# Kernel tuning notes

Hardware: AMD Instinct MI355X
Metric: run time of the kernel (lower is better)

## Reference

```python
import jax, jax.numpy as jnp
import numpy as np

DIM = 768
HID = 3072  # 4 * DIM
EPS = 1e-5


def layer_norm(x, w, b):
    mu = jnp.mean(x, axis=-1, keepdims=True)
    var = jnp.var(x, axis=-1, keepdims=True)
    return (x - mu) * jax.lax.rsqrt(var + EPS) * w + b


def setup_inputs() -> dict:
    key = jax.random.key(0)
    ks = jax.random.split(key, 8)
    C, H = DIM, HID
    s = lambda fan_in: 1.0 / np.sqrt(fan_in)
    return {
        "x": jax.random.normal(ks[0], (32, 577, C), dtype=jnp.float32),
        "norm1_w": jnp.ones((C,), jnp.float32),
        "norm1_b": jnp.zeros((C,), jnp.float32),
        "qkv_w": jax.random.uniform(ks[1], (3 * C, C), jnp.float32, -s(C), s(C)),
        "proj_w": jax.random.uniform(ks[2], (C, C), jnp.float32, -s(C), s(C)),
        "proj_b": jax.random.uniform(ks[3], (C,), jnp.float32, -s(C), s(C)),
        "norm2_w": jnp.ones((C,), jnp.float32),
        "norm2_b": jnp.zeros((C,), jnp.float32),
        "fc1_w": jax.random.uniform(ks[4], (H, C), jnp.float32, -s(C), s(C)),
        "fc1_b": jax.random.uniform(ks[5], (H,), jnp.float32, -s(C), s(C)),
        "fc2_w": jax.random.uniform(ks[6], (C, H), jnp.float32, -s(H), s(H)),
        "fc2_b": jax.random.uniform(ks[7], (C,), jnp.float32, -s(H), s(H)),
    }


def reference(x, norm1_w, norm1_b, qkv_w, proj_w, proj_b,
              norm2_w, norm2_b, fc1_w, fc1_b, fc2_w, fc2_b):
    B, N, C = x.shape
    attn_size = int((N - 1) ** 0.5)
    scale = C ** -0.5

    # --- Attention on norm1(x) (single head) ---
    h = layer_norm(x, norm1_w, norm1_b)
    qkv = (h @ qkv_w.T).reshape(B, N, 3, C)           # [B,N,3,C]
    q, k, v = qkv[:, :, 0], qkv[:, :, 1], qkv[:, :, 2]
    attn = jax.nn.softmax(jnp.einsum('bnc,bmc->bnm', q, k) * scale, axis=-1)
    y = jnp.einsum('bnm,bmc->bnc', attn, v)           # [B,N,C]
    # Faithful to torch: .transpose(1,2).reshape(B,N,C) scrambles layout
    y = jnp.transpose(y, (0, 2, 1)).reshape(B, N, C)
    a = y @ proj_w.T + proj_b
    token_attn = attn[:, 0, 1:].reshape(B, 1, attn_size, attn_size)

    # Faithful to torch Block: input residual is discarded, attention out doubled
    x = a + a

    # --- MLP (exact GELU, as nn.GELU default) ---
    m = layer_norm(x, norm2_w, norm2_b)
    m = jax.nn.gelu(m @ fc1_w.T + fc1_b, approximate=False)
    m = m @ fc2_w.T + fc2_b
    x = x + m
    return (x, token_attn)
```

## Files before the change

### kernel.cpp

```cpp
#include <hip/hip_runtime.h>
#include <hip/hip_bf16.h>

#define Bz   32
#define Nn_  577
#define Np   640
#define Cc   768
#define Hh   3072
#define Mrows (Bz * Nn_)
#define OUT_X (Mrows * Cc)
#define SCALE 0.03608439182435161f

typedef unsigned short ushort_t;
typedef short short8 __attribute__((ext_vector_type(8)));
typedef float f32x4 __attribute__((ext_vector_type(4)));

__device__ __forceinline__ ushort_t f2b(float f) {
    __hip_bfloat16 h = __float2bfloat16(f);
    return *reinterpret_cast<ushort_t*>(&h);
}

__device__ __forceinline__ void gl16(const ushort_t* g, ushort_t* l) {
    __builtin_amdgcn_global_load_lds(
        (const __attribute__((address_space(1))) void*)g,
        (__attribute__((address_space(3))) void*)l, 16, 0, 0);
}

__device__ __forceinline__ float bsum(float v, float* sm) {
    #pragma unroll
    for (int o = 32; o > 0; o >>= 1) v += __shfl_down(v, o, 64);
    int lane = threadIdx.x & 63, wid = threadIdx.x >> 6;
    if (lane == 0) sm[wid] = v;
    __syncthreads();
    float r = sm[0] + sm[1] + sm[2] + sm[3];
    __syncthreads();
    return r;
}
__device__ __forceinline__ float bmax(float v, float* sm) {
    #pragma unroll
    for (int o = 32; o > 0; o >>= 1) v = fmaxf(v, __shfl_down(v, o, 64));
    int lane = threadIdx.x & 63, wid = threadIdx.x >> 6;
    if (lane == 0) sm[wid] = v;
    __syncthreads();
    float r = fmaxf(fmaxf(sm[0], sm[1]), fmaxf(sm[2], sm[3]));
    __syncthreads();
    return r;
}

__global__ void cvt_kernel(const float* __restrict__ in, ushort_t* __restrict__ out, int n) {
    int i = blockIdx.x * 256 + threadIdx.x;
    if (i < n) out[i] = f2b(in[i]);
}

__global__ void ln_bf16(const float* __restrict__ x, const float* __restrict__ w,
                        const float* __restrict__ b, ushort_t* __restrict__ out) {
    __shared__ float sm[8];
    long long row = blockIdx.x;
    const float* xr = x + row * Cc;
    float v[3]; float s = 0.f;
    #pragma unroll
    for (int i = 0; i < 3; ++i) { v[i] = xr[threadIdx.x + i * 256]; s += v[i]; }
    float mu = bsum(s, sm) * (1.f / (float)Cc);
    float sq = 0.f;
    #pragma unroll
    for (int i = 0; i < 3; ++i) { float d = v[i] - mu; sq += d * d; }
    float var = bsum(sq, sm + 4) * (1.f / (float)Cc);
    float inv = rsqrtf(var + 1e-5f);
    ushort_t* orow = out + row * Cc;
    #pragma unroll
    for (int i = 0; i < 3; ++i) {
        int c = threadIdx.x + i * 256;
        orow[c] = f2b((v[i] - mu) * inv * w[c] + b[c]);
    }
}

__global__ void softmax_bf16(const float* __restrict__ Sf, ushort_t* __restrict__ Sb,
                             float* __restrict__ tok) {
    __shared__ float sm[8];
    long long row = blockIdx.x;
    int b_l = (int)(row / Nn_), r = (int)(row - (long long)b_l * Nn_);
    const float* src = Sf + row * Np;
    ushort_t* dst = Sb + row * Np;
    float v[3]; float mx = -1e30f;
    #pragma unroll
    for (int i = 0; i < 3; ++i) {
        int c = threadIdx.x + i * 256;
        v[i] = (c < Nn_) ? src[c] : -1e30f;
        mx = fmaxf(mx, v[i]);
    }
    mx = bmax(mx, sm);
    float s = 0.f;
    #pragma unroll
    for (int i = 0; i < 3; ++i) {
        int c = threadIdx.x + i * 256;
        v[i] = (c < Nn_) ? expf(v[i] - mx) : 0.f;
        s += v[i];
    }
    s = bsum(s, sm + 4);
    float inv = 1.f / s;
    #pragma unroll
    for (int i = 0; i < 3; ++i) {
        int c = threadIdx.x + i * 256;
        float p = v[i] * inv;
        if (c < Np) dst[c] = (c < Nn_) ? f2b(p) : (ushort_t)0;
        if (r == 0 && c >= 1 && c < Nn_) tok[(long long)b_l * 576 + (c - 1)] = p;
    }
}

#define EPS_STORE  0
#define EPS_X2     1
#define EPS_GELU   2
#define EPS_ADD    3
#define EPS_QKV    4

#define MM_STAGE(AS, BS, k0) do {            \
    gl16(Ag0 + (k0), &AS[e0]);               \
    gl16(Ag1 + (k0), &AS[e1]);               \
    gl16(Bg0 + (k0), &BS[e0]);               \
    gl16(Bg1 + (k0), &BS[e1]);               \
} while (0)

#define MM_COMPUTE(AS, BS) do {                                             \
    short8 af[4], bfr[4];                                                   \
    _Pragma("unroll")                                                       \
    for (int i = 0; i < 4; ++i) {                                           \
        int r = wr + i * 16 + fr;                                           \
        af[i] = *(const short8*)&AS[r * 32 + ((kq ^ (r & 3)) << 3)];        \
    }                                                                       \
    _Pragma("unroll")                                                       \
    for (int j = 0; j < 4; ++j) {                                           \
        int r = wc + j * 16 + fr;                                           \
        bfr[j] = *(const short8*)&BS[r * 32 + ((kq ^ (r & 3)) << 3)];       \
    }                                                                       \
    _Pragma("unroll")                                                       \
    for (int i = 0; i < 4; ++i)                                             \
        _Pragma("unroll")                                                   \
        for (int j = 0; j < 4; ++j)                                         \
            acc[i][j] = __builtin_amdgcn_mfma_f32_16x16x32_bf16(            \
                af[i], bfr[j], acc[i][j], 0, 0, 0);                         \
} while (0)

template<int EPI, typename OutT>
__global__ __launch_bounds__(256)
void mm_bf16(const ushort_t* __restrict__ A, long long sAb, int lda, int M,
             const ushort_t* __restrict__ B, long long sBb, int ldb, int Nv,
             const float* __restrict__ bias,
             OutT* __restrict__ O, long long sOb, int ldo,
             int K, float alpha,
             ushort_t* __restrict__ qQ, ushort_t* __restrict__ qK, ushort_t* __restrict__ qV)
{
    __shared__ __align__(16) ushort_t As0[128 * 32];
    __shared__ __align__(16) ushort_t As1[128 * 32];
    __shared__ __align__(16) ushort_t Bs0[128 * 32];
    __shared__ __align__(16) ushort_t Bs1[128 * 32];
    const int z = blockIdx.z;
    A += (long long)z * sAb; B += (long long)z * sBb;
    if (O) O += (long long)z * sOb;
    const int n0 = blockIdx.x * 128;
    const int m0 = blockIdx.y * 128;
    const int tid = threadIdx.x;
    const int lane = tid & 63;
    const int wv = tid >> 6;
    const int wr = (wv >> 1) << 6;
    const int wc = (wv & 1) << 6;
    const int fr = lane & 15;
    const int kq = lane >> 4;

    const int e0 = tid * 8, e1 = 2048 + tid * 8;
    const int ra0 = e0 >> 5, qa0 = (((e0 & 31) >> 3) ^ (ra0 & 3)) << 3;
    const int ra1 = e1 >> 5, qa1 = (((e1 & 31) >> 3) ^ (ra1 & 3)) << 3;
    const ushort_t* Ag0 = A + (long long)min(m0 + ra0, M - 1) * lda + qa0;
    const ushort_t* Ag1 = A + (long long)min(m0 + ra1, M - 1) * lda + qa1;
    const ushort_t* Bg0 = B + (long long)min(n0 + ra0, Nv - 1) * ldb + qa0;
    const ushort_t* Bg1 = B + (long long)min(n0 + ra1, Nv - 1) * ldb + qa1;

    f32x4 acc[4][4] = {};

    const int nt = K >> 5;

    MM_STAGE(As0, Bs0, 0);
    __syncthreads();

    for (int t = 0; t < nt; t += 2) {
        MM_STAGE(As1, Bs1, (t + 1) << 5);
        MM_COMPUTE(As0, Bs0);
        __syncthreads();
        if (t + 2 < nt) MM_STAGE(As0, Bs0, (t + 2) << 5);
        MM_COMPUTE(As1, Bs1);
        __syncthreads();
    }

    #pragma unroll
    for (int i = 0; i < 4; ++i) {
        int mb = m0 + wr + i * 16 + (lane >> 4) * 4;
        #pragma unroll
        for (int j = 0; j < 4; ++j) {
            int n = n0 + wc + j * 16 + fr;
            if (n >= Nv) continue;
            f32x4 v4 = acc[i][j];
            #pragma unroll
            for (int r = 0; r < 4; ++r) {
                int m = mb + r;
                if (m >= M) continue;
                float v = v4[r] * alpha;
                if constexpr (EPI == EPS_QKV) {
                    int b_l = m / Nn_, rr = m - b_l * Nn_;
                    if (n < Cc)            qQ[(long long)m * Cc + n] = f2b(v);
                    else if (n < 2 * Cc)   qK[(long long)m * Cc + (n - Cc)] = f2b(v);
                    else                   qV[((long long)b_l * Cc + (n - 2 * Cc)) * Np + rr] = f2b(v);
                } else if constexpr (EPI == EPS_ADD) {
                    if (bias) v += bias[n];
                    long long oi = (long long)m * ldo + n;
                    O[oi] += v;
                } else {
                    if (bias) v += bias[n];
                    if constexpr (EPI == EPS_X2) v *= 2.f;
                    if constexpr (EPI == EPS_GELU) v = 0.5f * v * (1.f + erff(v * 0.70710678118654752f));
                    long long oi = (long long)m * ldo + n;
                    if constexpr (sizeof(OutT) == 2) O[oi] = (OutT)f2b(v);
                    else                             O[oi] = (OutT)v;
                }
            }
        }
    }
}

extern "C" void kernel_launch(void* const* d_in, const int* in_sizes, int n_in,
                              void* d_out, int out_size, void* d_ws, size_t ws_size,
                              hipStream_t stream) {
    const float* x      = (const float*)d_in[0];
    const float* n1w    = (const float*)d_in[1];
    const float* n1b    = (const float*)d_in[2];
    const float* qkv_w  = (const float*)d_in[3];
    const float* proj_w = (const float*)d_in[4];
    const float* proj_b = (const float*)d_in[5];
    const float* n2w    = (const float*)d_in[6];
    const float* n2b    = (const float*)d_in[7];
    const float* fc1w   = (const float*)d_in[8];
    const float* fc1b   = (const float*)d_in[9];
    const float* fc2w   = (const float*)d_in[10];
    const float* fc2b   = (const float*)d_in[11];
    float* out = (float*)d_out;
    float* x2  = out;
    float* tok = out + OUT_X;

    char* ws = (char*)d_ws;
    const long long nWq = (long long)3 * Cc * Cc;
    const long long nWp = (long long)Cc * Cc;
    const long long nW1 = (long long)Hh * Cc;
    const long long nW2 = (long long)Cc * Hh;
    ushort_t* wq = (ushort_t*)ws;
    ushort_t* wp = wq + nWq;
    ushort_t* w1 = wp + nWp;
    ushort_t* w2 = w1 + nW1;
    const long long WBYTES = 2 * (nWq + nWp + nW1 + nW2);
    char* dyn = ws + WBYTES;
    long long avail = (long long)ws_size - WBYTES;

    const long long perG = 3LL * Nn_ * Cc * 2 + (long long)Cc * Np * 2
                         + (long long)Nn_ * Np * 4 + (long long)Nn_ * Np * 2;
    int G = 1;
    { const int o[6] = {32, 16, 8, 4, 2, 1};
      for (int i = 0; i < 6; ++i) if ((long long)o[i] * perG <= avail) { G = o[i]; break; } }
    int CH = Nn_;
    { const int o[6] = {32, 16, 8, 4, 2, 1};
      for (int i = 0; i < 6; ++i) if ((long long)o[i] * Nn_ * (Cc + Hh) * 2 <= avail) { CH = o[i] * Nn_; break; } }

    ushort_t* hbf = (ushort_t*)dyn;
    ushort_t* Q   = hbf + (long long)G * Nn_ * Cc;
    ushort_t* Kb  = Q   + (long long)G * Nn_ * Cc;
    ushort_t* Vt  = Kb  + (long long)G * Nn_ * Cc;
    float*    Sf  = (float*)(Vt + (long long)G * Cc * Np);
    ushort_t* Sb  = (ushort_t*)(Sf + (long long)G * Nn_ * Np);
    ushort_t* Yt  = hbf;
    ushort_t* g = (ushort_t*)dyn;
    ushort_t* t = g + (long long)CH * Cc;

    cvt_kernel<<<(int)((nWq + 255) / 256), 256, 0, stream>>>(qkv_w, wq, (int)nWq);
    cvt_kernel<<<(int)((nWp + 255) / 256), 256, 0, stream>>>(proj_w, wp, (int)nWp);
    cvt_kernel<<<(int)((nW1 + 255) / 256), 256, 0, stream>>>(fc1w, w1, (int)nW1);
    cvt_kernel<<<(int)((nW2 + 255) / 256), 256, 0, stream>>>(fc2w, w2, (int)nW2);

    for (int b0 = 0; b0 < Bz; b0 += G) {
        const int MR = G * Nn_;
        const int myM = (MR + 127) / 128;

        ln_bf16<<<MR, 256, 0, stream>>>(x + (long long)b0 * Nn_ * Cc, n1w, n1b, hbf);

        mm_bf16<EPS_QKV, float><<<dim3(18, myM, 1), 256, 0, stream>>>(
            hbf, 0, Cc, MR, wq, 0, Cc, 3 * Cc, nullptr,
            (float*)nullptr, 0, 0, Cc, 1.f, Q, Kb, Vt);

        mm_bf16<EPS_STORE, float><<<dim3(5, 5, G), 256, 0, stream>>>(
            Q, (long long)Nn_ * Cc, Cc, Nn_, Kb, (long long)Nn_ * Cc, Cc, Nn_, nullptr,
            Sf, (long long)Nn_ * Np, Np, Cc, SCALE, nullptr, nullptr, nullptr);

        softmax_bf16<<<MR, 256, 0, stream>>>(Sf, Sb, tok + (long long)b0 * 576);

        mm_bf16<EPS_STORE, ushort_t><<<dim3(5, 6, G), 256, 0, stream>>>(
            Vt, (long long)Cc * Np, Np, Cc, Sb, (long long)Nn_ * Np, Np, Nn_, nullptr,
            Yt, (long long)Cc * Nn_, Nn_, Np, 1.f, nullptr, nullptr, nullptr);

        mm_bf16<EPS_X2, float><<<dim3(6, myM, 1), 256, 0, stream>>>(
            Yt, 0, Cc, MR, wp, 0, Cc, Cc, proj_b,
            x2 + (long long)b0 * Nn_ * Cc, 0, Cc, Cc, 1.f, nullptr, nullptr, nullptr);
    }

    for (int c0 = 0; c0 < Mrows; c0 += CH) {
        const int cn = (Mrows - c0 < CH) ? (Mrows - c0) : CH;
        const int myC = (cn + 127) / 128;

        ln_bf16<<<cn, 256, 0, stream>>>(x2 + (long long)c0 * Cc, n2w, n2b, g);

        mm_bf16<EPS_GELU, ushort_t><<<dim3(24, myC, 1), 256, 0, stream>>>(
            g, 0, Cc, cn, w1, 0, Cc, Hh, fc1b,
            t, 0, Hh, Cc, 1.f, nullptr, nullptr, nullptr);

        mm_bf16<EPS_ADD, float><<<dim3(6, myC, 1), 256, 0, stream>>>(
            t, 0, Hh, cn, w2, 0, Hh, Cc, fc2b,
            x2 + (long long)c0 * Cc, 0, Cc, Hh, 1.f, nullptr, nullptr, nullptr);
    }
}
```

Baseline: 890.0 us.

## Add 256x256 double-buffered MFMA GEMM kernel for dense projections

Introduces mm256, a 512-thread GEMM with 256x256 output tiles and two LDS buffers. Global-to-LDS loads for the next K tile are issued before computing the current one, with a swizzled LDS layout, s_setprio around the MFMA bursts and an XCD-aware workgroup remap. It replaces the 128-tile mm_bf16 for the QKV, proj, fc1 and fc2 GEMMs to raise data reuse per tile and overlap loads with compute. In exchange it uses 128KB of LDS per block, limiting occupancy to one block per CU, and launches far fewer workgroups, which can leave CUs underused on the smaller GEMMs.

Result: faster. 872.1 us (-2.0%).

```diff
diff --git a/kernel.cpp b/kernel.cpp
--- a/kernel.cpp
+++ b/kernel.cpp
@@ -224,6 +224,144 @@
     }
 }
 
+#define STAGE256(LA, LB, kt) do {                                   \
+    _Pragma("unroll")                                               \
+    for (int j = 0; j < 4; ++j) gl16(Ag[j] + (kt) * 64, &LA[j * 4096 + sdst]); \
+    _Pragma("unroll")                                               \
+    for (int j = 0; j < 4; ++j) gl16(Bg[j] + (kt) * 64, &LB[j * 4096 + sdst]); \
+} while (0)
+
+#define COMPUTE256(LA, LB) do {                                                   \
+    short8 bfv[4][2];                                                             \
+    _Pragma("unroll")                                                             \
+    for (int nf = 0; nf < 4; ++nf) {                                              \
+        int rb = (wn64 + nf * 16 + fr) * 64;                                      \
+        bfv[nf][0] = *(const short8*)&LB[rb + ck0];                               \
+        bfv[nf][1] = *(const short8*)&LB[rb + ck1];                               \
+    }                                                                             \
+    _Pragma("unroll")                                                             \
+    for (int mh = 0; mh < 4; ++mh) {                                              \
+        int ra0 = (wm128 + mh * 32 + fr) * 64;                                    \
+        int ra1 = (wm128 + mh * 32 + 16 + fr) * 64;                               \
+        short8 a00 = *(const short8*)&LA[ra0 + ck0];                              \
+        short8 a01 = *(const short8*)&LA[ra0 + ck1];                              \
+        short8 a10 = *(const short8*)&LA[ra1 + ck0];                              \
+        short8 a11 = *(const short8*)&LA[ra1 + ck1];                              \
+        __builtin_amdgcn_s_setprio(1);                                            \
+        _Pragma("unroll")                                                         \
+        for (int nf = 0; nf < 4; ++nf) {                                          \
+            acc[mh*2][nf]   = __builtin_amdgcn_mfma_f32_16x16x32_bf16(a00, bfv[nf][0], acc[mh*2][nf],   0,0,0); \
+            acc[mh*2][nf]   = __builtin_amdgcn_mfma_f32_16x16x32_bf16(a01, bfv[nf][1], acc[mh*2][nf],   0,0,0); \
+            acc[mh*2+1][nf] = __builtin_amdgcn_mfma_f32_16x16x32_bf16(a10, bfv[nf][0], acc[mh*2+1][nf], 0,0,0); \
+            acc[mh*2+1][nf] = __builtin_amdgcn_mfma_f32_16x16x32_bf16(a11, bfv[nf][1], acc[mh*2+1][nf], 0,0,0); \
+        }                                                                         \
+        __builtin_amdgcn_s_setprio(0);                                            \
+    }                                                                             \
+} while (0)
+
+#define TILE_STEP256(RA, RB, WA, WB, kt) do {                       \
+    if ((kt) + 1 < nt) {                                            \
+        STAGE256(WA, WB, (kt) + 1);                                 \
+        asm volatile("s_waitcnt vmcnt(8)" ::: "memory");            \
+    } else {                                                        \
+        asm volatile("s_waitcnt vmcnt(0)" ::: "memory");            \
+    }                                                               \
+    __builtin_amdgcn_s_barrier();                                   \
+    __builtin_amdgcn_sched_barrier(0);                              \
+    COMPUTE256(RA, RB);                                             \
+    __builtin_amdgcn_s_barrier();                                   \
+    __builtin_amdgcn_sched_barrier(0);                              \
+} while (0)
+
+template<int EPI, typename OutT>
+__global__ __launch_bounds__(512, 2)
+void mm256(const ushort_t* __restrict__ A, int lda, int M,
+           const ushort_t* __restrict__ B, int ldb, int Nv,
+           const float* __restrict__ bias,
+           OutT* __restrict__ O, int ldo,
+           int K, float alpha,
+           ushort_t* __restrict__ qQ, ushort_t* __restrict__ qK, ushort_t* __restrict__ qV)
+{
+    __shared__ __align__(16) ushort_t As0[256 * 64];
+    __shared__ __align__(16) ushort_t Bs0[256 * 64];
+    __shared__ __align__(16) ushort_t As1[256 * 64];
+    __shared__ __align__(16) ushort_t Bs1[256 * 64];
+
+    const int nwg = gridDim.x * gridDim.y;
+    const int flat = blockIdx.y * gridDim.x + blockIdx.x;
+    const int qq = nwg >> 3, rr8 = nwg & 7;
+    const int xcd = flat & 7, idx = flat >> 3;
+    const int wg = (xcd < rr8 ? xcd * (qq + 1) : rr8 * (qq + 1) + (xcd - rr8) * qq) + idx;
+    const int bx = wg % gridDim.x, by = wg / gridDim.x;
+
+    const int n0 = bx * 256, m0 = by * 256;
+    const int tid = (int)threadIdx.x;
+    const int lane = tid & 63;
+    const int wv = tid >> 6;
+    const int wm128 = (wv >> 2) * 128;
+    const int wn64  = (wv & 3) * 64;
+    const int fr = lane & 15;
+    const int kq = lane >> 4;
+    const int f7 = fr & 7;
+    const int ck0 = (kq ^ f7) * 8;
+    const int ck1 = ((4 + kq) ^ f7) * 8;
+
+    const int srow = tid >> 3;
+    const int schunk = (tid & 7) ^ (srow & 7);
+    const int sdst = tid * 8;
+    const ushort_t* Ag[4];
+    const ushort_t* Bg[4];
+    #pragma unroll
+    for (int j = 0; j < 4; ++j) {
+        Ag[j] = A + (long long)min(m0 + j * 64 + srow, M - 1) * lda + schunk * 8;
+        Bg[j] = B + (long long)min(n0 + j * 64 + srow, Nv - 1) * ldb + schunk * 8;
+    }
+
+    f32x4 acc[8][4] = {};
+    const int nt = K >> 6;
+
+    STAGE256(As0, Bs0, 0);
+
+    for (int t = 0; t < nt; t += 2) {
+        TILE_STEP256(As0, Bs0, As1, Bs1, t);
+        TILE_STEP256(As1, Bs1, As0, Bs0, t + 1);
+    }
+
+    #pragma unroll
+    for (int mf = 0; mf < 8; ++mf) {
+        int mb = m0 + wm128 + mf * 16 + (lane >> 4) * 4;
+        #pragma unroll
+        for (int nf = 0; nf < 4; ++nf) {
+            int n = n0 + wn64 + nf * 16 + fr;
+            if (n >= Nv) continue;
+            f32x4 v4 = acc[mf][nf];
+            #pragma unroll
+            for (int r = 0; r < 4; ++r) {
+                int m = mb + r;
+                if (m >= M) continue;
+                float v = v4[r] * alpha;
+                if constexpr (EPI == EPS_QKV) {
+                    int b_l = m / Nn_, rq = m - b_l * Nn_;
+                    if (n < Cc)            qQ[(long long)m * Cc + n] = f2b(v);
+                    else if (n < 2 * Cc)   qK[(long long)m * Cc + (n - Cc)] = f2b(v);
+                    else                   qV[((long long)b_l * Cc + (n - 2 * Cc)) * Np + rq] = f2b(v);
+                } else if constexpr (EPI == EPS_ADD) {
+                    if (bias) v += bias[n];
+                    long long oi = (long long)m * ldo + n;
+                    O[oi] += v;
+                } else {
+                    if (bias) v += bias[n];
+                    if constexpr (EPI == EPS_X2) v *= 2.f;
+                    if constexpr (EPI == EPS_GELU) v = 0.5f * v * (1.f + erff(v * 0.70710678118654752f));
+                    long long oi = (long long)m * ldo + n;
+                    if constexpr (sizeof(OutT) == 2) O[oi] = (OutT)f2b(v);
+                    else                             O[oi] = (OutT)v;
+                }
+            }
+        }
+    }
+}
+
 extern "C" void kernel_launch(void* const* d_in, const int* in_sizes, int n_in,
                               void* d_out, int out_size, void* d_ws, size_t ws_size,
                               hipStream_t stream) {
@@ -282,13 +420,13 @@
 
     for (int b0 = 0; b0 < Bz; b0 += G) {
         const int MR = G * Nn_;
-        const int myM = (MR + 127) / 128;
+        const int myM256 = (MR + 255) / 256;
 
         ln_bf16<<<MR, 256, 0, stream>>>(x + (long long)b0 * Nn_ * Cc, n1w, n1b, hbf);
 
-        mm_bf16<EPS_QKV, float><<<dim3(18, myM, 1), 256, 0, stream>>>(
-            hbf, 0, Cc, MR, wq, 0, Cc, 3 * Cc, nullptr,
-            (float*)nullptr, 0, 0, Cc, 1.f, Q, Kb, Vt);
+        mm256<EPS_QKV, float><<<dim3(9, myM256, 1), 512, 0, stream>>>(
+            hbf, Cc, MR, wq, Cc, 3 * Cc, nullptr,
+            (float*)nullptr, 0, Cc, 1.f, Q, Kb, Vt);
 
         mm_bf16<EPS_STORE, float><<<dim3(5, 5, G), 256, 0, stream>>>(
             Q, (long long)Nn_ * Cc, Cc, Nn_, Kb, (long long)Nn_ * Cc, Cc, Nn_, nullptr,
@@ -300,23 +438,23 @@
             Vt, (long long)Cc * Np, Np, Cc, Sb, (long long)Nn_ * Np, Np, Nn_, nullptr,
             Yt, (long long)Cc * Nn_, Nn_, Np, 1.f, nullptr, nullptr, nullptr);
 
-        mm_bf16<EPS_X2, float><<<dim3(6, myM, 1), 256, 0, stream>>>(
-            Yt, 0, Cc, MR, wp, 0, Cc, Cc, proj_b,
-            x2 + (long long)b0 * Nn_ * Cc, 0, Cc, Cc, 1.f, nullptr, nullptr, nullptr);
+        mm256<EPS_X2, float><<<dim3(3, myM256, 1), 512, 0, stream>>>(
+            Yt, Cc, MR, wp, Cc, Cc, proj_b,
+            x2 + (long long)b0 * Nn_ * Cc, Cc, Cc, 1.f, nullptr, nullptr, nullptr);
     }
 
     for (int c0 = 0; c0 < Mrows; c0 += CH) {
         const int cn = (Mrows - c0 < CH) ? (Mrows - c0) : CH;
-        const int myC = (cn + 127) / 128;
+        const int myC256 = (cn + 255) / 256;
 
         ln_bf16<<<cn, 256, 0, stream>>>(x2 + (long long)c0 * Cc, n2w, n2b, g);
 
-        mm_bf16<EPS_GELU, ushort_t><<<dim3(24, myC, 1), 256, 0, stream>>>(
-            g, 0, Cc, cn, w1, 0, Cc, Hh, fc1b,
-            t, 0, Hh, Cc, 1.f, nullptr, nullptr, nullptr);
-
-        mm_bf16<EPS_ADD, float><<<dim3(6, myC, 1), 256, 0, stream>>>(
-            t, 0, Hh, cn, w2, 0, Hh, Cc, fc2b,
-            x2 + (long long)c0 * Cc, 0, Cc, Hh, 1.f, nullptr, nullptr, nullptr);
-    }
-}
+        mm256<EPS_GELU, ushort_t><<<dim3(12, myC256, 1), 512, 0, stream>>>(
+            g, Cc, cn, w1, Cc, Hh, fc1b,
+            t, Hh, Cc, 1.f, nullptr, nullptr, nullptr);
+
+        mm256<EPS_ADD, float><<<dim3(3, myC256, 1), 512, 0, stream>>>(
+            t, Hh, cn, w2, Hh, Cc, fc2b,
+            x2 + (long long)c0 * Cc, Cc, Hh, 1.f, nullptr, nullptr, nullptr);
+    }
+}
```
